# Optimization experiments

Hardware: AMD Instinct MI355X
Metric: run time of the kernel (lower is better)

The kernel has to match this reference:

```python
import jax, jax.numpy as jnp
import numpy as np

BLOCK_SIZE = 2048
FRAMES = 4096
BASE_RESONANCE = 0.5
MAX_GAIN = 5.0


def fft_convolve(a, b):
    # Linear convolution via zero-padded FFT, truncated to original length
    # (matches the matching-pursuit repo's fft_convolve).
    n = a.shape[-1]
    fa = jnp.fft.rfft(a, n=2 * n, axis=-1)
    fb = jnp.fft.rfft(b, n=2 * n, axis=-1)
    out = jnp.fft.irfft(fa * fb, n=2 * n, axis=-1)
    return out[..., :n]


def setup_inputs() -> dict:
    key = jax.random.key(0)
    ks = jax.random.split(key, 6)
    cp = jax.random.normal(ks[0], (1, BLOCK_SIZE, FRAMES), dtype=jnp.float32)
    w1 = jax.random.uniform(ks[1], (BLOCK_SIZE, BLOCK_SIZE), jnp.float32, -0.01, 0.01)
    w2 = jax.random.uniform(ks[2], (BLOCK_SIZE, BLOCK_SIZE), jnp.float32, -0.01, 0.01)
    audio = jax.random.uniform(ks[3], (BLOCK_SIZE, BLOCK_SIZE), jnp.float32, -0.01, 0.01)
    decays = jax.random.uniform(ks[4], (BLOCK_SIZE,), jnp.float32, 0.001, 0.99)
    gains = jax.random.uniform(ks[5], (BLOCK_SIZE,), jnp.float32, -3.0, 3.0)
    return {"cp": cp, "w1": w1, "w2": w2, "audio": audio, "decays": decays, "gains": gains}


def reference(cp, w1, w2, audio, decays, gains):
    b, c, frames = cp.shape  # b == 1, c == BLOCK_SIZE
    x0 = jnp.maximum(cp, 0.0)  # torch.relu(cp)
    # decay values in (base_resonance, 1): base + sigmoid(decays) * span
    d = BASE_RESONANCE + jax.nn.sigmoid(decays) * (1.0 - BASE_RESONANCE)  # (c,)
    g = jax.nn.sigmoid(gains) * MAX_GAIN  # (c,)

    x = jnp.einsum('ij,bjt->bit', w1, x0)  # mapping @ control_plane
    orig = x

    # decay envelope: log -> cumsum -> exp over frames => d ** (t+1)
    logd = jnp.log(1e-12 + jnp.broadcast_to(d[None, :, None], (b, c, frames)))
    denv = jnp.exp(jnp.cumsum(logd, axis=-1))  # (b, c, frames)

    x = fft_convolve(x, denv)
    x = jnp.einsum('ij,bjt->bit', w2, x) + orig
    cp_out = jnp.tanh(x * g[None, :, None])

    audio_out = jnp.einsum('wj,bjt->bwt', audio, cp_out)  # (b, window, frames)
    audio_out = jnp.transpose(audio_out, (0, 2, 1)).reshape(b, 1, -1)
    return audio_out, cp_out
```

## Files before the change

kernel.cpp:

```cpp
#include <hip/hip_runtime.h>
#include <math.h>

typedef __attribute__((ext_vector_type(8))) short bf16x8;
typedef __attribute__((ext_vector_type(8))) unsigned short u16x8;
typedef __attribute__((ext_vector_type(4))) unsigned short u16x4;
typedef __attribute__((ext_vector_type(4))) float f32x4;
typedef unsigned short u16;

__device__ __forceinline__ u16 f2bf(float f) {
  unsigned u = __builtin_bit_cast(unsigned, f);
  return (u16)((u + 0x7FFFu + ((u >> 16) & 1u)) >> 16);
}

__device__ __forceinline__ void gload16(const u16* g, u16* l) {
  __builtin_amdgcn_global_load_lds((const __attribute__((address_space(1))) void*)g,
                                   (__attribute__((address_space(3))) void*)l, 16, 0, 0);
}

__device__ __forceinline__ void sbar() {
  __builtin_amdgcn_sched_barrier(0);
  __builtin_amdgcn_s_barrier();
  __builtin_amdgcn_sched_barrier(0);
}

#define VMWAIT(n) asm volatile("s_waitcnt vmcnt(" #n ")" ::: "memory")
#define MFMA16(a, b, c) __builtin_amdgcn_mfma_f32_16x16x32_bf16((a), (b), (c), 0, 0, 0)

__device__ __forceinline__ float decay_of(float d) {
  return 1e-12f + 0.5f + 0.5f / (1.0f + expf(-d));
}

__global__ __launch_bounds__(256) void cvt_bf16_kernel(const float* __restrict__ in,
                                                       u16* __restrict__ out, int n4) {
  int i = blockIdx.x * 256 + threadIdx.x;
  if (i >= n4) return;
  const float4 v = ((const float4*)in)[i];
  u16x4 o = { f2bf(v.x), f2bf(v.y), f2bf(v.z), f2bf(v.w) };
  ((u16x4*)out)[i] = o;
}

__global__ __launch_bounds__(256) void relu_t_kernel(const float* __restrict__ cp,
                                                     u16* __restrict__ x0t) {
  const int cb = blockIdx.x & 31;
  const int tb = blockIdx.x >> 5;
  __shared__ __attribute__((aligned(16))) float tile[64][65];
  const int tid = threadIdx.x;
  const int r0 = tid >> 4, i4 = (tid & 15) * 4;
  #pragma unroll
  for (int rr = 0; rr < 64; rr += 16) {
    const float4 v = *(const float4*)(cp + (size_t)(cb * 64 + r0 + rr) * 4096 + tb * 64 + i4);
    tile[r0 + rr][i4 + 0] = fmaxf(v.x, 0.f);
    tile[r0 + rr][i4 + 1] = fmaxf(v.y, 0.f);
    tile[r0 + rr][i4 + 2] = fmaxf(v.z, 0.f);
    tile[r0 + rr][i4 + 3] = fmaxf(v.w, 0.f);
  }
  __syncthreads();
  #pragma unroll
  for (int it = 0; it < 2; ++it) {
    const int chunk = it * 256 + tid;
    const int i = chunk >> 3, rp = (chunk & 7) * 8;
    u16x8 o;
    #pragma unroll
    for (int q = 0; q < 8; ++q) o[q] = f2bf(tile[rp + q][i]);
    *(u16x8*)(x0t + (size_t)(tb * 64 + i) * 2048 + cb * 64 + rp) = o;
  }
}

__global__ __launch_bounds__(128) void iir_partial_kernel(const float* __restrict__ x,
                                                          const float* __restrict__ decays,
                                                          float* __restrict__ L) {
  const int tid = threadIdx.x;
  const int cb = blockIdx.x & 15;
  const int ck = blockIdx.x >> 4;
  const int c0 = cb * 128, t0 = ck * 64;
  __shared__ __attribute__((aligned(16))) float xs[128][65];
  const float dd = decay_of(decays[c0 + tid]);
  #pragma unroll
  for (int it = 0; it < 16; ++it) {
    const int idx = it * 128 + tid;
    const int r = idx >> 4, iv = (idx & 15) * 4;
    const float4 v = *(const float4*)(x + (size_t)(c0 + r) * 4096 + t0 + iv);
    xs[r][iv + 0] = v.x; xs[r][iv + 1] = v.y; xs[r][iv + 2] = v.z; xs[r][iv + 3] = v.w;
  }
  __syncthreads();
  float yv = 0.0f;
  #pragma unroll
  for (int i = 0; i < 64; ++i) yv = dd * (xs[tid][i] + yv);
  L[ck * 2048 + c0 + tid] = yv;
}

__global__ __launch_bounds__(128) void iir_carry_kernel(const float* __restrict__ L,
                                                        const float* __restrict__ decays,
                                                        float* __restrict__ Cin) {
  const int c = blockIdx.x * 128 + threadIdx.x;
  const float dd = decay_of(decays[c]);
  float A = dd;
  #pragma unroll
  for (int p = 0; p < 6; ++p) A = A * A;
  float carry = 0.0f;
  for (int j = 0; j < 64; ++j) {
    Cin[j * 2048 + c] = carry;
    carry = L[j * 2048 + c] + A * carry;
  }
}

__global__ __launch_bounds__(128) void iir_apply_kernel(const float* __restrict__ x,
                                                        const float* __restrict__ decays,
                                                        const float* __restrict__ Cin,
                                                        u16* __restrict__ yT) {
  const int tid = threadIdx.x;
  const int cb = blockIdx.x & 15;
  const int ck = blockIdx.x >> 4;
  const int c0 = cb * 128, t0 = ck * 64;
  __shared__ __attribute__((aligned(16))) float xs[128][65];
  __shared__ __attribute__((aligned(16))) u16 ys[64][136];
  const float dd = decay_of(decays[c0 + tid]);
  const float carry = Cin[ck * 2048 + c0 + tid];
  #pragma unroll
  for (int it = 0; it < 16; ++it) {
    const int idx = it * 128 + tid;
    const int r = idx >> 4, iv = (idx & 15) * 4;
    const float4 v = *(const float4*)(x + (size_t)(c0 + r) * 4096 + t0 + iv);
    xs[r][iv + 0] = v.x; xs[r][iv + 1] = v.y; xs[r][iv + 2] = v.z; xs[r][iv + 3] = v.w;
  }
  __syncthreads();
  float yv = carry;
  #pragma unroll
  for (int i = 0; i < 64; ++i) {
    yv = dd * (xs[tid][i] + yv);
    ys[i][tid] = f2bf(yv);
  }
  __syncthreads();
  #pragma unroll
  for (int it = 0; it < 8; ++it) {
    const int chunk = it * 128 + tid;
    const int i = chunk >> 4, cpv = (chunk & 15) * 8;
    u16x8 v = *(const u16x8*)&ys[i][cpv];
    *(u16x8*)(yT + (size_t)(t0 + i) * 2048 + c0 + cpv) = v;
  }
}

template <int MODE>
__global__ __launch_bounds__(256, 2) void gemm_db_kernel(
    const u16* __restrict__ A, const u16* __restrict__ Bt, float* __restrict__ C,
    int N, int K, int xlogn,
    const float* __restrict__ orig, const float* __restrict__ gains,
    u16* __restrict__ CbT) {
  __shared__ __attribute__((aligned(16))) u16 Asb[2][128 * 64];
  __shared__ __attribute__((aligned(16))) u16 Bsb[2][128 * 64];
  const int tid = threadIdx.x;
  const int l = tid & 63, w = tid >> 6;
  const int xc = blockIdx.x & 7, rblk = blockIdx.x >> 3;
  const int xn = xc & ((1 << xlogn) - 1), xm = xc >> xlogn;
  const int bm = xm * 8 + (rblk >> 3);
  const int bn = xn * 8 + (rblk & 7);
  const int nt = K >> 6;

  const int cs = (l & 7) ^ (l >> 3);
  const int rsub = l >> 3;
  const u16* aS[4]; const u16* bS[4]; int tO[4];
  #pragma unroll
  for (int u = 0; u < 4; ++u) {
    const int rg = (u * 4 + w) * 8 + rsub;
    aS[u] = A  + (size_t)(bm * 128 + rg) * K + cs * 8;
    bS[u] = Bt + (size_t)(bn * 128 + rg) * K + cs * 8;
    tO[u] = (u * 4 + w) * 512;
  }

#define STAGE(bufA, bufB, tt) do {                                        \
    const long so_ = (long)(tt) * 64;                                     \
    gload16(aS[0] + so_, (bufA) + tO[0]); gload16(aS[1] + so_, (bufA) + tO[1]); \
    gload16(aS[2] + so_, (bufA) + tO[2]); gload16(aS[3] + so_, (bufA) + tO[3]); \
    gload16(bS[0] + so_, (bufB) + tO[0]); gload16(bS[1] + so_, (bufB) + tO[1]); \
    gload16(bS[2] + so_, (bufB) + tO[2]); gload16(bS[3] + so_, (bufB) + tO[3]); \
  } while (0)

  STAGE((u16*)Asb[0], (u16*)Bsb[0], 0);
  STAGE((u16*)Asb[1], (u16*)Bsb[1], 1);

  f32x4 acc[4][4];
  #pragma unroll
  for (int i = 0; i < 4; ++i)
    #pragma unroll
    for (int j = 0; j < 4; ++j) acc[i][j] = (f32x4){0.f, 0.f, 0.f, 0.f};

  const int wr = w >> 1, wc = w & 1;
  const int rA0 = wr * 64 + (l & 15);
  const int rB0 = wc * 64 + (l & 15);
  const int jk0 = (l >> 4) ^ (l & 7);
  const int jk1 = ((l >> 4) + 4) ^ (l & 7);

  VMWAIT(8);
  sbar();

  for (int t = 0; t < nt; ++t) {
    const u16* Ac = Asb[t & 1];
    const u16* Bc = Bsb[t & 1];
    bf16x8 a0[4], b0[4], a1[4], b1[4];
    #pragma unroll
    for (int mi = 0; mi < 4; ++mi)
      a0[mi] = *(const bf16x8*)(Ac + (rA0 + mi * 16) * 64 + jk0 * 8);
    #pragma unroll
    for (int ni = 0; ni < 4; ++ni)
      b0[ni] = *(const bf16x8*)(Bc + (rB0 + ni * 16) * 64 + jk0 * 8);
    #pragma unroll
    for (int mi = 0; mi < 4; ++mi)
      a1[mi] = *(const bf16x8*)(Ac + (rA0 + mi * 16) * 64 + jk1 * 8);
    #pragma unroll
    for (int ni = 0; ni < 4; ++ni)
      b1[ni] = *(const bf16x8*)(Bc + (rB0 + ni * 16) * 64 + jk1 * 8);
    __builtin_amdgcn_s_setprio(1);
    #pragma unroll
    for (int mi = 0; mi < 4; ++mi)
      #pragma unroll
      for (int ni = 0; ni < 4; ++ni)
        acc[mi][ni] = MFMA16(a0[mi], b0[ni], acc[mi][ni]);
    #pragma unroll
    for (int mi = 0; mi < 4; ++mi)
      #pragma unroll
      for (int ni = 0; ni < 4; ++ni)
        acc[mi][ni] = MFMA16(a1[mi], b1[ni], acc[mi][ni]);
    __builtin_amdgcn_s_setprio(0);
    sbar();
    if (t + 2 < nt) {
      STAGE((u16*)Asb[t & 1], (u16*)Bsb[t & 1], t + 2);
      VMWAIT(8);
    } else if (t + 1 < nt) {
      VMWAIT(0);
    }
    sbar();
  }
#undef STAGE

  const int rb = bm * 128 + wr * 64 + ((l >> 4) * 4);
  const int cb = bn * 128 + wc * 64 + (l & 15);
  #pragma unroll
  for (int mi = 0; mi < 4; ++mi) {
    const int row0 = rb + mi * 16;
    float gv[4] = {0.f, 0.f, 0.f, 0.f};
    if (MODE == 1) {
      #pragma unroll
      for (int j = 0; j < 4; ++j) gv[j] = 5.0f / (1.0f + expf(-gains[row0 + j]));
    }
    #pragma unroll
    for (int ni = 0; ni < 4; ++ni) {
      const int col = cb + ni * 16;
      f32x4 v = acc[mi][ni];
      if (MODE == 1) {
        float cpv[4];
        #pragma unroll
        for (int j = 0; j < 4; ++j) {
          float t = v[j] + orig[(size_t)(row0 + j) * N + col];
          cpv[j] = tanhf(t * gv[j]);
          C[(size_t)(row0 + j) * N + col] = cpv[j];
        }
        u16x4 o = { f2bf(cpv[0]), f2bf(cpv[1]), f2bf(cpv[2]), f2bf(cpv[3]) };
        *(u16x4*)(CbT + (size_t)col * 2048 + row0) = o;
      } else {
        #pragma unroll
        for (int j = 0; j < 4; ++j)
          C[(size_t)(row0 + j) * N + col] = v[j];
      }
    }
  }
}

extern "C" void kernel_launch(void* const* d_in, const int* in_sizes, int n_in,
                              void* d_out, int out_size, void* d_ws, size_t ws_size,
                              hipStream_t stream) {
  const float* cp     = (const float*)d_in[0];
  const float* w1     = (const float*)d_in[1];
  const float* w2     = (const float*)d_in[2];
  const float* audio  = (const float*)d_in[3];
  const float* decays = (const float*)d_in[4];
  const float* gains  = (const float*)d_in[5];

  float* out0 = (float*)d_out;
  float* out1 = out0 + (size_t)2048 * 4096;

  char* ws = (char*)d_ws;
  u16*   w1b    = (u16*)(ws);
  u16*   w2b    = (u16*)(ws + 8388608);
  u16*   audiob = (u16*)(ws + 16777216);
  float* orig   = (float*)(ws + 25165824);
  u16*   yT     = (u16*)(ws + 58720256);
  u16*   x0t    = (u16*)(ws + 75497472);
  u16*   cpbT   = x0t;
  float* Lbuf   = (float*)(ws + 75497472);
  float* Cin    = (float*)(ws + 75497472 + 524288);

  cvt_bf16_kernel<<<4096, 256, 0, stream>>>(w1, w1b, 1048576);
  cvt_bf16_kernel<<<4096, 256, 0, stream>>>(w2, w2b, 1048576);
  cvt_bf16_kernel<<<4096, 256, 0, stream>>>(audio, audiob, 1048576);
  relu_t_kernel<<<2048, 256, 0, stream>>>(cp, x0t);

  gemm_db_kernel<0><<<512, 256, 0, stream>>>(w1b, x0t, orig, 4096, 2048, 2,
                                             nullptr, nullptr, nullptr);
  iir_partial_kernel<<<1024, 128, 0, stream>>>(orig, decays, Lbuf);
  iir_carry_kernel<<<16, 128, 0, stream>>>(Lbuf, decays, Cin);
  iir_apply_kernel<<<1024, 128, 0, stream>>>(orig, decays, Cin, yT);
  gemm_db_kernel<1><<<512, 256, 0, stream>>>(w2b, yT, out1, 4096, 2048, 2,
                                             orig, gains, cpbT);
  gemm_db_kernel<0><<<512, 256, 0, stream>>>(cpbT, audiob, out0, 2048, 2048, 1,
                                             nullptr, nullptr, nullptr);
}
```

Before: 187.5 us.

## Load GEMM A operand directly from global into registers, fuse bf16 conversions

The GEMM kernel no longer stages the A operand through LDS. Each lane now loads its A fragments straight from global memory into registers, with an even/odd register double buffer, while B stays double-buffered in LDS. This halves LDS footprint and traffic and removes the A-side global-to-LDS copies, at the cost of uncoalesced 16-byte global reads per lane and more VGPR pressure. The three weight fp32-to-bf16 conversions are also merged into one launch writing a contiguous buffer, relying on w1b, w2b and audiob being adjacent in the workspace.

```diff
diff --git a/kernel.cpp b/kernel.cpp
--- a/kernel.cpp
+++ b/kernel.cpp
@@ -30,11 +30,17 @@
   return 1e-12f + 0.5f + 0.5f / (1.0f + expf(-d));
 }
 
-__global__ __launch_bounds__(256) void cvt_bf16_kernel(const float* __restrict__ in,
-                                                       u16* __restrict__ out, int n4) {
-  int i = blockIdx.x * 256 + threadIdx.x;
-  if (i >= n4) return;
-  const float4 v = ((const float4*)in)[i];
+__global__ __launch_bounds__(256) void cvt3_kernel(const float* __restrict__ a,
+                                                   const float* __restrict__ b,
+                                                   const float* __restrict__ c,
+                                                   u16* __restrict__ out) {
+  const int i = blockIdx.x * 256 + threadIdx.x;
+  const float* src;
+  int j = i;
+  if (i < 1048576) { src = a; }
+  else if (i < 2097152) { src = b; j = i - 1048576; }
+  else { src = c; j = i - 2097152; }
+  const float4 v = ((const float4*)src)[j];
   u16x4 o = { f2bf(v.x), f2bf(v.y), f2bf(v.z), f2bf(v.w) };
   ((u16x4*)out)[i] = o;
 }
@@ -140,13 +146,48 @@
   }
 }
 
+__device__ __forceinline__ void load_a(const u16* aBase, long koff, long K,
+                                       bf16x8 (&a0)[4], bf16x8 (&a1)[4]) {
+  #pragma unroll
+  for (int mi = 0; mi < 4; ++mi) {
+    a0[mi] = *(const bf16x8*)(aBase + (size_t)mi * 16 * K + koff);
+    a1[mi] = *(const bf16x8*)(aBase + (size_t)mi * 16 * K + koff + 32);
+  }
+}
+
+__device__ __forceinline__ void read_b(const u16* Bc, int rB0, int jk0, int jk1,
+                                       bf16x8 (&b0)[4], bf16x8 (&b1)[4]) {
+  #pragma unroll
+  for (int ni = 0; ni < 4; ++ni)
+    b0[ni] = *(const bf16x8*)(Bc + (rB0 + ni * 16) * 64 + jk0 * 8);
+  #pragma unroll
+  for (int ni = 0; ni < 4; ++ni)
+    b1[ni] = *(const bf16x8*)(Bc + (rB0 + ni * 16) * 64 + jk1 * 8);
+}
+
+__device__ __forceinline__ void do_mfma(const bf16x8 (&a0)[4], const bf16x8 (&a1)[4],
+                                        const bf16x8 (&b0)[4], const bf16x8 (&b1)[4],
+                                        f32x4 (&acc)[4][4]) {
+  __builtin_amdgcn_s_setprio(1);
+  #pragma unroll
+  for (int mi = 0; mi < 4; ++mi)
+    #pragma unroll
+    for (int ni = 0; ni < 4; ++ni)
+      acc[mi][ni] = MFMA16(a0[mi], b0[ni], acc[mi][ni]);
+  #pragma unroll
+  for (int mi = 0; mi < 4; ++mi)
+    #pragma unroll
+    for (int ni = 0; ni < 4; ++ni)
+      acc[mi][ni] = MFMA16(a1[mi], b1[ni], acc[mi][ni]);
+  __builtin_amdgcn_s_setprio(0);
+}
+
 template <int MODE>
-__global__ __launch_bounds__(256, 2) void gemm_db_kernel(
+__global__ __launch_bounds__(256, 2) void gemm_ad_kernel(
     const u16* __restrict__ A, const u16* __restrict__ Bt, float* __restrict__ C,
     int N, int K, int xlogn,
     const float* __restrict__ orig, const float* __restrict__ gains,
     u16* __restrict__ CbT) {
-  __shared__ __attribute__((aligned(16))) u16 Asb[2][128 * 64];
   __shared__ __attribute__((aligned(16))) u16 Bsb[2][128 * 64];
   const int tid = threadIdx.x;
   const int l = tid & 63, w = tid >> 6;
@@ -158,31 +199,19 @@
 
   const int cs = (l & 7) ^ (l >> 3);
   const int rsub = l >> 3;
-  const u16* aS[4]; const u16* bS[4]; int tO[4];
+  const u16* bS[4]; int tO[4];
   #pragma unroll
   for (int u = 0; u < 4; ++u) {
     const int rg = (u * 4 + w) * 8 + rsub;
-    aS[u] = A  + (size_t)(bm * 128 + rg) * K + cs * 8;
     bS[u] = Bt + (size_t)(bn * 128 + rg) * K + cs * 8;
     tO[u] = (u * 4 + w) * 512;
   }
 
-#define STAGE(bufA, bufB, tt) do {                                        \
-    const long so_ = (long)(tt) * 64;                                     \
-    gload16(aS[0] + so_, (bufA) + tO[0]); gload16(aS[1] + so_, (bufA) + tO[1]); \
-    gload16(aS[2] + so_, (bufA) + tO[2]); gload16(aS[3] + so_, (bufA) + tO[3]); \
-    gload16(bS[0] + so_, (bufB) + tO[0]); gload16(bS[1] + so_, (bufB) + tO[1]); \
-    gload16(bS[2] + so_, (bufB) + tO[2]); gload16(bS[3] + so_, (bufB) + tO[3]); \
+#define STAGEB(buf, tt) do {                                               \
+    const long so_ = (long)(tt) * 64;                                      \
+    gload16(bS[0] + so_, (buf) + tO[0]); gload16(bS[1] + so_, (buf) + tO[1]); \
+    gload16(bS[2] + so_, (buf) + tO[2]); gload16(bS[3] + so_, (buf) + tO[3]); \
   } while (0)
-
-  STAGE((u16*)Asb[0], (u16*)Bsb[0], 0);
-  STAGE((u16*)Asb[1], (u16*)Bsb[1], 1);
-
-  f32x4 acc[4][4];
-  #pragma unroll
-  for (int i = 0; i < 4; ++i)
-    #pragma unroll
-    for (int j = 0; j < 4; ++j) acc[i][j] = (f32x4){0.f, 0.f, 0.f, 0.f};
 
   const int wr = w >> 1, wc = w & 1;
   const int rA0 = wr * 64 + (l & 15);
@@ -190,47 +219,40 @@
   const int jk0 = (l >> 4) ^ (l & 7);
   const int jk1 = ((l >> 4) + 4) ^ (l & 7);
 
-  VMWAIT(8);
+  const u16* aBase = A + (size_t)(bm * 128 + rA0) * K + (l >> 4) * 8;
+
+  f32x4 acc[4][4];
+  #pragma unroll
+  for (int i = 0; i < 4; ++i)
+    #pragma unroll
+    for (int j = 0; j < 4; ++j) acc[i][j] = (f32x4){0.f, 0.f, 0.f, 0.f};
+
+  bf16x8 aE0[4], aE1[4], aO0[4], aO1[4], b0[4], b1[4];
+
+  load_a(aBase, 0, K, aE0, aE1);
+  STAGEB((u16*)Bsb[0], 0);
+  STAGEB((u16*)Bsb[1], 1);
+  VMWAIT(4);
   sbar();
 
-  for (int t = 0; t < nt; ++t) {
-    const u16* Ac = Asb[t & 1];
-    const u16* Bc = Bsb[t & 1];
-    bf16x8 a0[4], b0[4], a1[4], b1[4];
-    #pragma unroll
-    for (int mi = 0; mi < 4; ++mi)
-      a0[mi] = *(const bf16x8*)(Ac + (rA0 + mi * 16) * 64 + jk0 * 8);
-    #pragma unroll
-    for (int ni = 0; ni < 4; ++ni)
-      b0[ni] = *(const bf16x8*)(Bc + (rB0 + ni * 16) * 64 + jk0 * 8);
-    #pragma unroll
-    for (int mi = 0; mi < 4; ++mi)
-      a1[mi] = *(const bf16x8*)(Ac + (rA0 + mi * 16) * 64 + jk1 * 8);
-    #pragma unroll
-    for (int ni = 0; ni < 4; ++ni)
-      b1[ni] = *(const bf16x8*)(Bc + (rB0 + ni * 16) * 64 + jk1 * 8);
-    __builtin_amdgcn_s_setprio(1);
-    #pragma unroll
-    for (int mi = 0; mi < 4; ++mi)
-      #pragma unroll
-      for (int ni = 0; ni < 4; ++ni)
-        acc[mi][ni] = MFMA16(a0[mi], b0[ni], acc[mi][ni]);
-    #pragma unroll
-    for (int mi = 0; mi < 4; ++mi)
-      #pragma unroll
-      for (int ni = 0; ni < 4; ++ni)
-        acc[mi][ni] = MFMA16(a1[mi], b1[ni], acc[mi][ni]);
-    __builtin_amdgcn_s_setprio(0);
+  for (int t = 0; t < nt; t += 2) {
+    const bool more = (t + 2) < nt;
+    load_a(aBase, (long)(t + 1) * 64, K, aO0, aO1);
+    read_b((const u16*)Bsb[0], rB0, jk0, jk1, b0, b1);
+    do_mfma(aE0, aE1, b0, b1, acc);
     sbar();
-    if (t + 2 < nt) {
-      STAGE((u16*)Asb[t & 1], (u16*)Bsb[t & 1], t + 2);
-      VMWAIT(8);
-    } else if (t + 1 < nt) {
-      VMWAIT(0);
-    }
+    if (more) { STAGEB((u16*)Bsb[0], t + 2); VMWAIT(4); }
+    else      { VMWAIT(0); }
     sbar();
-  }
-#undef STAGE
+    if (more) load_a(aBase, (long)(t + 2) * 64, K, aE0, aE1);
+    read_b((const u16*)Bsb[1], rB0, jk0, jk1, b0, b1);
+    do_mfma(aO0, aO1, b0, b1, acc);
+    sbar();
+    if (more) { STAGEB((u16*)Bsb[1], t + 3); VMWAIT(4); }
+    else      { VMWAIT(0); }
+    sbar();
+  }
+#undef STAGEB
 
   const int rb = bm * 128 + wr * 64 + ((l >> 4) * 4);
   const int cb = bn * 128 + wc * 64 + (l & 15);
@@ -289,18 +311,16 @@
   float* Lbuf   = (float*)(ws + 75497472);
   float* Cin    = (float*)(ws + 75497472 + 524288);
 
-  cvt_bf16_kernel<<<4096, 256, 0, stream>>>(w1, w1b, 1048576);
-  cvt_bf16_kernel<<<4096, 256, 0, stream>>>(w2, w2b, 1048576);
-  cvt_bf16_kernel<<<4096, 256, 0, stream>>>(audio, audiob, 1048576);
+  cvt3_kernel<<<12288, 256, 0, stream>>>(w1, w2, audio, w1b);
   relu_t_kernel<<<2048, 256, 0, stream>>>(cp, x0t);
 
-  gemm_db_kernel<0><<<512, 256, 0, stream>>>(w1b, x0t, orig, 4096, 2048, 2,
+  gemm_ad_kernel<0><<<512, 256, 0, stream>>>(w1b, x0t, orig, 4096, 2048, 2,
                                              nullptr, nullptr, nullptr);
   iir_partial_kernel<<<1024, 128, 0, stream>>>(orig, decays, Lbuf);
   iir_carry_kernel<<<16, 128, 0, stream>>>(Lbuf, decays, Cin);
   iir_apply_kernel<<<1024, 128, 0, stream>>>(orig, decays, Cin, yT);
-  gemm_db_kernel<1><<<512, 256, 0, stream>>>(w2b, yT, out1, 4096, 2048, 2,
+  gemm_ad_kernel<1><<<512, 256, 0, stream>>>(w2b, yT, out1, 4096, 2048, 2,
                                              orig, gains, cpbT);
-  gemm_db_kernel<0><<<512, 256, 0, stream>>>(cpbT, audiob, out0, 2048, 2048, 1,
+  gemm_ad_kernel<0><<<512, 256, 0, stream>>>(cpbT, audiob, out0, 2048, 2048, 1,
                                              nullptr, nullptr, nullptr);
 }
```

Result: slower. 294.9 us (+57.2%).

## Software-pipeline LDS fragment reads in GEMM and fuse three bf16 conversions

Applied to the files above, without the earlier changes.

Restructures the GEMM main loop so the first half-K fragment of the next tile is read from LDS before the loop iteration, overlapping LDS reads with MFMA work. The barrier count per iteration drops from two to one, at the cost of a full vmcnt(0) wait before the barrier, which may expose global-load latency. The three weight conversion launches are merged into one kernel that writes contiguous workspace buffers, relying on w1b, w2b and audiob being adjacent.

```diff
diff --git a/kernel.cpp b/kernel.cpp
--- a/kernel.cpp
+++ b/kernel.cpp
@@ -30,11 +30,17 @@
   return 1e-12f + 0.5f + 0.5f / (1.0f + expf(-d));
 }
 
-__global__ __launch_bounds__(256) void cvt_bf16_kernel(const float* __restrict__ in,
-                                                       u16* __restrict__ out, int n4) {
-  int i = blockIdx.x * 256 + threadIdx.x;
-  if (i >= n4) return;
-  const float4 v = ((const float4*)in)[i];
+__global__ __launch_bounds__(256) void cvt3_kernel(const float* __restrict__ a,
+                                                   const float* __restrict__ b,
+                                                   const float* __restrict__ c,
+                                                   u16* __restrict__ out) {
+  const int i = blockIdx.x * 256 + threadIdx.x;
+  const float* src;
+  int j = i;
+  if (i < 1048576) { src = a; }
+  else if (i < 2097152) { src = b; j = i - 1048576; }
+  else { src = c; j = i - 2097152; }
+  const float4 v = ((const float4*)src)[j];
   u16x4 o = { f2bf(v.x), f2bf(v.y), f2bf(v.z), f2bf(v.w) };
   ((u16x4*)out)[i] = o;
 }
@@ -140,8 +146,30 @@
   }
 }
 
+__device__ __forceinline__ void read_frag(const u16* Ac, const u16* Bc,
+                                          int rA0, int rB0, int jk,
+                                          bf16x8 (&a)[4], bf16x8 (&b)[4]) {
+  #pragma unroll
+  for (int i = 0; i < 4; ++i)
+    a[i] = *(const bf16x8*)(Ac + (rA0 + i * 16) * 64 + jk * 8);
+  #pragma unroll
+  for (int i = 0; i < 4; ++i)
+    b[i] = *(const bf16x8*)(Bc + (rB0 + i * 16) * 64 + jk * 8);
+}
+
+__device__ __forceinline__ void mfma16x(const bf16x8 (&a)[4], const bf16x8 (&b)[4],
+                                        f32x4 (&acc)[4][4]) {
+  __builtin_amdgcn_s_setprio(1);
+  #pragma unroll
+  for (int mi = 0; mi < 4; ++mi)
+    #pragma unroll
+    for (int ni = 0; ni < 4; ++ni)
+      acc[mi][ni] = MFMA16(a[mi], b[ni], acc[mi][ni]);
+  __builtin_amdgcn_s_setprio(0);
+}
+
 template <int MODE>
-__global__ __launch_bounds__(256, 2) void gemm_db_kernel(
+__global__ __launch_bounds__(256, 2) void gemm_pl_kernel(
     const u16* __restrict__ A, const u16* __restrict__ Bt, float* __restrict__ C,
     int N, int K, int xlogn,
     const float* __restrict__ orig, const float* __restrict__ gains,
@@ -190,45 +218,27 @@
   const int jk0 = (l >> 4) ^ (l & 7);
   const int jk1 = ((l >> 4) + 4) ^ (l & 7);
 
+  bf16x8 pa[4], pb[4], qa[4], qb[4];
+
   VMWAIT(8);
   sbar();
-
-  for (int t = 0; t < nt; ++t) {
-    const u16* Ac = Asb[t & 1];
-    const u16* Bc = Bsb[t & 1];
-    bf16x8 a0[4], b0[4], a1[4], b1[4];
-    #pragma unroll
-    for (int mi = 0; mi < 4; ++mi)
-      a0[mi] = *(const bf16x8*)(Ac + (rA0 + mi * 16) * 64 + jk0 * 8);
-    #pragma unroll
-    for (int ni = 0; ni < 4; ++ni)
-      b0[ni] = *(const bf16x8*)(Bc + (rB0 + ni * 16) * 64 + jk0 * 8);
-    #pragma unroll
-    for (int mi = 0; mi < 4; ++mi)
-      a1[mi] = *(const bf16x8*)(Ac + (rA0 + mi * 16) * 64 + jk1 * 8);
-    #pragma unroll
-    for (int ni = 0; ni < 4; ++ni)
-      b1[ni] = *(const bf16x8*)(Bc + (rB0 + ni * 16) * 64 + jk1 * 8);
-    __builtin_amdgcn_s_setprio(1);
-    #pragma unroll
-    for (int mi = 0; mi < 4; ++mi)
-      #pragma unroll
-      for (int ni = 0; ni < 4; ++ni)
-        acc[mi][ni] = MFMA16(a0[mi], b0[ni], acc[mi][ni]);
-    #pragma unroll
-    for (int mi = 0; mi < 4; ++mi)
-      #pragma unroll
-      for (int ni = 0; ni < 4; ++ni)
-        acc[mi][ni] = MFMA16(a1[mi], b1[ni], acc[mi][ni]);
-    __builtin_amdgcn_s_setprio(0);
+  read_frag((const u16*)Asb[0], (const u16*)Bsb[0], rA0, rB0, jk0, pa, pb);
+
+  for (int h = 0; h < nt; ++h) {
+    const u16* Ac = (const u16*)Asb[0] + (h & 1) * 8192;
+    const u16* Bc = (const u16*)Bsb[0] + (h & 1) * 8192;
+    u16* Anx = (u16*)Asb[0] + (h & 1) * 8192;
+    u16* Bnx = (u16*)Bsb[0] + (h & 1) * 8192;
+    const u16* An1 = (const u16*)Asb[0] + ((h + 1) & 1) * 8192;
+    const u16* Bn1 = (const u16*)Bsb[0] + ((h + 1) & 1) * 8192;
+
+    read_frag(Ac, Bc, rA0, rB0, jk1, qa, qb);
+    mfma16x(pa, pb, acc);
+    mfma16x(qa, qb, acc);
+    VMWAIT(0);
     sbar();
-    if (t + 2 < nt) {
-      STAGE((u16*)Asb[t & 1], (u16*)Bsb[t & 1], t + 2);
-      VMWAIT(8);
-    } else if (t + 1 < nt) {
-      VMWAIT(0);
-    }
-    sbar();
+    if (h + 2 < nt) STAGE(Anx, Bnx, h + 2);
+    if (h + 1 < nt) read_frag(An1, Bn1, rA0, rB0, jk0, pa, pb);
   }
 #undef STAGE
 
@@ -289,18 +299,16 @@
   float* Lbuf   = (float*)(ws + 75497472);
   float* Cin    = (float*)(ws + 75497472 + 524288);
 
-  cvt_bf16_kernel<<<4096, 256, 0, stream>>>(w1, w1b, 1048576);
-  cvt_bf16_kernel<<<4096, 256, 0, stream>>>(w2, w2b, 1048576);
-  cvt_bf16_kernel<<<4096, 256, 0, stream>>>(audio, audiob, 1048576);
+  cvt3_kernel<<<12288, 256, 0, stream>>>(w1, w2, audio, w1b);
   relu_t_kernel<<<2048, 256, 0, stream>>>(cp, x0t);
 
-  gemm_db_kernel<0><<<512, 256, 0, stream>>>(w1b, x0t, orig, 4096, 2048, 2,
+  gemm_pl_kernel<0><<<512, 256, 0, stream>>>(w1b, x0t, orig, 4096, 2048, 2,
                                              nullptr, nullptr, nullptr);
   iir_partial_kernel<<<1024, 128, 0, stream>>>(orig, decays, Lbuf);
   iir_carry_kernel<<<16, 128, 0, stream>>>(Lbuf, decays, Cin);
   iir_apply_kernel<<<1024, 128, 0, stream>>>(orig, decays, Cin, yT);
-  gemm_db_kernel<1><<<512, 256, 0, stream>>>(w2b, yT, out1, 4096, 2048, 2,
+  gemm_pl_kernel<1><<<512, 256, 0, stream>>>(w2b, yT, out1, 4096, 2048, 2,
                                              orig, gains, cpbT);
-  gemm_db_kernel<0><<<512, 256, 0, stream>>>(cpbT, audiob, out0, 2048, 2048, 1,
+  gemm_pl_kernel<0><<<512, 256, 0, stream>>>(cpbT, audiob, out0, 2048, 2048, 1,
                                              nullptr, nullptr, nullptr);
 }
```

Result: no change. 186.5 us (-0.6%).
